# Kernel optimization log

Measured on AMD Instinct MI355X. Metric: run time of the kernel, lower is better.

The kernel has to match this reference:

```python
import jax, jax.numpy as jnp
import numpy as np

T, N = 512, 256          # timesteps, parallel envs
STATE, HID = 64, 128     # input features, GRU hidden size


def setup_inputs() -> dict:
    key = jax.random.key(0)
    k = jax.random.split(key, 6)
    inputs = jax.random.normal(k[0], (T * N, STATE), dtype=jnp.float32)
    hxs = jax.random.normal(k[1], (N, HID), dtype=jnp.float32)
    masks = (jax.random.uniform(k[2], (T * N, 1)) > 0.02).astype(jnp.float32)
    # GRU params (torch layout: gates ordered r, z, n; rows = 3*HID)
    weight_ih = jax.random.normal(k[3], (3 * HID, STATE), dtype=jnp.float32) * 0.1
    weight_hh = jax.random.normal(k[4], (3 * HID, HID), dtype=jnp.float32) * 0.1
    bias_ih = jnp.zeros((3 * HID,), dtype=jnp.float32)  # init.constant_(0)
    bias_hh = jnp.zeros((3 * HID,), dtype=jnp.float32)
    return {
        "inputs": inputs, "hxs": hxs, "masks": masks,
        "weight_ih": weight_ih, "weight_hh": weight_hh,
        "bias_ih": bias_ih, "bias_hh": bias_hh,
    }


def reference(inputs, hxs, masks, weight_ih, weight_hh, bias_ih, bias_hh):
    n, hid = hxs.shape
    t = inputs.shape[0] // n
    x = inputs.reshape(t, n, -1)       # (t, n, state)
    m = masks.reshape(t, n, 1)         # (t, n, 1)

    # Input-to-gate projections are mask-independent: precompute for all steps.
    gx = jnp.einsum('tns,gs->tng', x, weight_ih) + bias_ih  # (t, n, 3H)

    def step(h, xs):
        gx_t, m_t = xs
        h = h * m_t                                 # inline reset (fused; replaces chunk splitting)
        gh = h @ weight_hh.T + bias_hh              # (n, 3H)
        xr, xz, xn = jnp.split(gx_t, 3, axis=-1)
        hr, hz, hn = jnp.split(gh, 3, axis=-1)
        r = jax.nn.sigmoid(xr + hr)
        z = jax.nn.sigmoid(xz + hz)
        cand = jnp.tanh(xn + r * hn)
        h = (1.0 - z) * cand + z * h                # torch GRU update
        return h, h

    h_final, ys = jax.lax.scan(step, hxs, (gx, m))  # ys: (t, n, H)
    return ys.reshape(t * n, hid), h_final
```

## Files before the change

### kernel.cpp

```cpp
#include <hip/hip_runtime.h>
#include <math.h>

#define T_STEPS  512
#define N_ENVS   256
#define STATE    64
#define HID      128
#define NTHREADS 512

typedef _Float16 half8   __attribute__((ext_vector_type(8)));
typedef _Float16 half4_t __attribute__((ext_vector_type(4)));
typedef float    floatx4 __attribute__((ext_vector_type(4)));

__device__ __forceinline__ float sigmoid_fast(float v) {
    return __builtin_amdgcn_rcpf(1.f + __expf(-v));
}
__device__ __forceinline__ float tanh_fast(float v) {
    const float e  = __expf(-2.f * fabsf(v));
    const float mg = (1.f - e) * __builtin_amdgcn_rcpf(1.f + e);
    return copysignf(mg, v);
}

__global__ __launch_bounds__(NTHREADS, 2) void gru_mfma_split(
    const float* __restrict__ x,
    const float* __restrict__ h0,
    const float* __restrict__ masks,
    const float* __restrict__ wih,
    const float* __restrict__ whh,
    const float* __restrict__ bih,
    const float* __restrict__ bhh,
    float* __restrict__ out)
{
    const int b    = blockIdx.x;
    const int tid  = threadIdx.x;
    const int w    = tid >> 6;
    const int lane = tid & 63;
    const int c    = lane & 15;
    const int quad = lane >> 4;
    const int j    = 16 * w + c;

    __shared__ __align__(16) _Float16 buf[2][HID];
    __shared__ __align__(16) _Float16 xh[2][16][STATE];
    __shared__ __align__(16) float    gxp[16][HID][4];
    __shared__ __align__(16) float    ring[2][16][HID];
    __shared__ float ms[32];

    const int rowb[3] = { j, HID + j, 2 * HID + j };
    half8 Bh[3][4];
#pragma unroll
    for (int ti = 0; ti < 3; ++ti) {
        const int g = rowb[ti];
#pragma unroll
        for (int kt = 0; kt < 4; ++kt) {
            const float* src = whh + (size_t)g * HID + kt * 32 + quad * 8;
            const float4 p0 = *(const float4*)(src);
            const float4 p1 = *(const float4*)(src + 4);
            half8 hb;
            hb[0] = (_Float16)p0.x; hb[1] = (_Float16)p0.y;
            hb[2] = (_Float16)p0.z; hb[3] = (_Float16)p0.w;
            hb[4] = (_Float16)p1.x; hb[5] = (_Float16)p1.y;
            hb[6] = (_Float16)p1.z; hb[7] = (_Float16)p1.w;
            Bh[ti][kt] = hb;
        }
    }
    half8 Bx[3][2];
#pragma unroll
    for (int ti = 0; ti < 3; ++ti) {
        const int g = rowb[ti];
#pragma unroll
        for (int kt = 0; kt < 2; ++kt) {
            const float* src = wih + (size_t)g * STATE + kt * 32 + quad * 8;
            const float4 p0 = *(const float4*)(src);
            const float4 p1 = *(const float4*)(src + 4);
            half8 hb;
            hb[0] = (_Float16)p0.x; hb[1] = (_Float16)p0.y;
            hb[2] = (_Float16)p0.z; hb[3] = (_Float16)p0.w;
            hb[4] = (_Float16)p1.x; hb[5] = (_Float16)p1.y;
            hb[6] = (_Float16)p1.z; hb[7] = (_Float16)p1.w;
            Bx[ti][kt] = hb;
        }
    }

    const float br  = bih[j] + bhh[j];
    const float bz  = bih[HID + j] + bhh[HID + j];
    const float bhn = bhh[2 * HID + j];
    const float bxn = bih[2 * HID + j];

    float hr = h0[(size_t)b * HID + j];
    const float m0 = masks[b];
    float hm = m0 * hr;
    if (quad == 0) buf[0][j] = (_Float16)hm;

    float4 xp = {0.f, 0.f, 0.f, 0.f};
    if (tid < 256) {
        const int k = tid >> 4, cc = (tid & 15) * 4;
        const float4 xv = *(const float4*)(x + ((size_t)k * N_ENVS + b) * STATE + cc);
        half4_t hx = {(_Float16)xv.x, (_Float16)xv.y, (_Float16)xv.z, (_Float16)xv.w};
        *(half4_t*)&xh[0][k][cc] = hx;
        xp = *(const float4*)(x + ((size_t)(16 + k) * N_ENVS + b) * STATE + cc);
    }
    float mreg = 0.f;
    if (tid < 16) {
        ms[tid] = masks[(size_t)tid * N_ENVS + b];
        mreg = masks[(size_t)(16 + tid) * N_ENVS + b];
    }
    __syncthreads();

    const floatx4 zero4 = {0.f, 0.f, 0.f, 0.f};

    for (int tc = 0; tc < 32; ++tc) {
        if (tc > 0) {
            const int k = tid >> 5, jj = (tid & 31) * 4;
            *(float4*)(out + ((size_t)((tc - 1) * 16 + k) * N_ENVS + b) * HID + jj) =
                *(const float4*)&ring[(tc - 1) & 1][k][jj];
        }
        if (tid < 256) {
            const int k = tid >> 4, cc = (tid & 15) * 4;
            half4_t hx = {(_Float16)xp.x, (_Float16)xp.y, (_Float16)xp.z, (_Float16)xp.w};
            *(half4_t*)&xh[(tc + 1) & 1][k][cc] = hx;
            const int st = (tc + 2) * 16 + k;
            if (st < T_STEPS)
                xp = *(const float4*)(x + ((size_t)st * N_ENVS + b) * STATE + cc);
        }
        if (tid < 16) {
            ms[(tc * 16 + 16 + tid) & 31] = mreg;
            const int st = tc * 16 + 32 + tid;
            if (st < T_STEPS) mreg = masks[(size_t)st * N_ENVS + b];
        }

        {
            const _Float16* xr = &xh[tc & 1][c][0];
            half8 ax0 = *(const half8*)&xr[quad * 8];
            half8 ax1 = *(const half8*)&xr[32 + quad * 8];
            floatx4 g0 = __builtin_amdgcn_mfma_f32_16x16x32_f16(ax0, Bx[0][0], zero4, 0, 0, 0);
            floatx4 g1 = __builtin_amdgcn_mfma_f32_16x16x32_f16(ax0, Bx[1][0], zero4, 0, 0, 0);
            floatx4 g2 = __builtin_amdgcn_mfma_f32_16x16x32_f16(ax0, Bx[2][0], zero4, 0, 0, 0);
            g0 = __builtin_amdgcn_mfma_f32_16x16x32_f16(ax1, Bx[0][1], g0, 0, 0, 0);
            g1 = __builtin_amdgcn_mfma_f32_16x16x32_f16(ax1, Bx[1][1], g1, 0, 0, 0);
            g2 = __builtin_amdgcn_mfma_f32_16x16x32_f16(ax1, Bx[2][1], g2, 0, 0, 0);
#pragma unroll
            for (int i = 0; i < 4; ++i) {
                const int s4 = quad * 4 + i;
                gxp[s4][j][0] = g0[i];
                gxp[s4][j][1] = g1[i];
                gxp[s4][j][2] = g2[i];
            }
        }
        __syncthreads();

#pragma unroll
        for (int s = 0; s < 16; ++s) {
            const int t = tc * 16 + s;
            const _Float16* bufc = buf[s & 1];
            _Float16* bufn = (_Float16*)buf[(s + 1) & 1];

            half8 a0 = *(const half8*)(bufc + 0 * 32 + quad * 8);
            half8 a1 = *(const half8*)(bufc + 1 * 32 + quad * 8);
            half8 a2 = *(const half8*)(bufc + 2 * 32 + quad * 8);
            half8 a3 = *(const half8*)(bufc + 3 * 32 + quad * 8);

            floatx4 r_a = __builtin_amdgcn_mfma_f32_16x16x32_f16(a0, Bh[0][0], zero4, 0, 0, 0);
            floatx4 r_b = __builtin_amdgcn_mfma_f32_16x16x32_f16(a2, Bh[0][2], zero4, 0, 0, 0);
            floatx4 z_a = __builtin_amdgcn_mfma_f32_16x16x32_f16(a0, Bh[1][0], zero4, 0, 0, 0);
            floatx4 z_b = __builtin_amdgcn_mfma_f32_16x16x32_f16(a2, Bh[1][2], zero4, 0, 0, 0);
            floatx4 n_a = __builtin_amdgcn_mfma_f32_16x16x32_f16(a0, Bh[2][0], zero4, 0, 0, 0);
            floatx4 n_b = __builtin_amdgcn_mfma_f32_16x16x32_f16(a2, Bh[2][2], zero4, 0, 0, 0);
            r_a = __builtin_amdgcn_mfma_f32_16x16x32_f16(a1, Bh[0][1], r_a, 0, 0, 0);
            r_b = __builtin_amdgcn_mfma_f32_16x16x32_f16(a3, Bh[0][3], r_b, 0, 0, 0);
            z_a = __builtin_amdgcn_mfma_f32_16x16x32_f16(a1, Bh[1][1], z_a, 0, 0, 0);
            z_b = __builtin_amdgcn_mfma_f32_16x16x32_f16(a3, Bh[1][3], z_b, 0, 0, 0);
            n_a = __builtin_amdgcn_mfma_f32_16x16x32_f16(a1, Bh[2][1], n_a, 0, 0, 0);
            n_b = __builtin_amdgcn_mfma_f32_16x16x32_f16(a3, Bh[2][3], n_b, 0, 0, 0);

            const float4 gx4 = *(const float4*)&gxp[s][j][0];

            const float ur = (r_a[0] + r_b[0]) + gx4.x + br;
            const float uz = (z_a[0] + z_b[0]) + gx4.y + bz;
            const float hn = (n_a[0] + n_b[0]) + bhn;
            const float xn = gx4.z + bxn;
            const float r  = sigmoid_fast(ur);
            const float z  = sigmoid_fast(uz);
            const float cd = tanh_fast(fmaf(r, hn, xn));
            const float hnew = fmaf(z, hm - cd, cd);

            if (quad == 0) ring[tc & 1][s][j] = hnew;
            if (t < T_STEPS - 1) {
                const float mn = ms[(t + 1) & 31];
                hm = mn * hnew;
                if (quad == 0) bufn[j] = (_Float16)hm;
            }
            hr = hnew;
            __syncthreads();
        }
    }

    {
        const int k = tid >> 5, jj = (tid & 31) * 4;
        *(float4*)(out + ((size_t)(496 + k) * N_ENVS + b) * HID + jj) =
            *(const float4*)&ring[1][k][jj];
    }
    if (quad == 0)
        out[(size_t)T_STEPS * N_ENVS * HID + (size_t)b * HID + j] = hr;
}

extern "C" void kernel_launch(void* const* d_in, const int* in_sizes, int n_in,
                              void* d_out, int out_size, void* d_ws, size_t ws_size,
                              hipStream_t stream) {
    const float* x   = (const float*)d_in[0];
    const float* h0  = (const float*)d_in[1];
    const float* mk  = (const float*)d_in[2];
    const float* wih = (const float*)d_in[3];
    const float* whh = (const float*)d_in[4];
    const float* bih = (const float*)d_in[5];
    const float* bhh = (const float*)d_in[6];
    float* out = (float*)d_out;

    hipLaunchKernelGGL(gru_mfma_split, dim3(N_ENVS), dim3(NTHREADS), 0, stream,
                       x, h0, mk, wih, whh, bih, bhh, out);
}
```

Measured before the change: 305.1 us.

## Keep masks and outputs in registers, pack gate preacts to fp16, fuse activations

Masks move from shared memory into per-lane registers and are read with readlane, and the outputs are buffered in registers instead of an LDS ring. Each quad keeps its own four timesteps and writes them out per chunk with scalar stores. The input-gate preactivations are stored as fp16 with the biases folded in, halving LDS traffic. The xh rows are padded to reduce bank conflicts. The sigmoid/tanh/update sequence is fused into one reciprocal, shortening the serial per-step chain, at the cost of fp16 precision on the input gates and less coalesced output stores.

```diff
diff --git a/kernel.cpp b/kernel.cpp
--- a/kernel.cpp
+++ b/kernel.cpp
@@ -6,21 +6,13 @@
 #define STATE    64
 #define HID      128
 #define NTHREADS 512
+#define XPAD     72
 
 typedef _Float16 half8   __attribute__((ext_vector_type(8)));
 typedef _Float16 half4_t __attribute__((ext_vector_type(4)));
 typedef float    floatx4 __attribute__((ext_vector_type(4)));
 
-__device__ __forceinline__ float sigmoid_fast(float v) {
-    return __builtin_amdgcn_rcpf(1.f + __expf(-v));
-}
-__device__ __forceinline__ float tanh_fast(float v) {
-    const float e  = __expf(-2.f * fabsf(v));
-    const float mg = (1.f - e) * __builtin_amdgcn_rcpf(1.f + e);
-    return copysignf(mg, v);
-}
-
-__global__ __launch_bounds__(NTHREADS, 2) void gru_mfma_split(
+__global__ __launch_bounds__(NTHREADS, 2) void gru_r6(
     const float* __restrict__ x,
     const float* __restrict__ h0,
     const float* __restrict__ masks,
@@ -39,10 +31,8 @@
     const int j    = 16 * w + c;
 
     __shared__ __align__(16) _Float16 buf[2][HID];
-    __shared__ __align__(16) _Float16 xh[2][16][STATE];
-    __shared__ __align__(16) float    gxp[16][HID][4];
-    __shared__ __align__(16) float    ring[2][16][HID];
-    __shared__ float ms[32];
+    __shared__ __align__(16) _Float16 xh[2][16][XPAD];
+    __shared__ __align__(16) _Float16 gxp[16][HID][4];
 
     const int rowb[3] = { j, HID + j, 2 * HID + j };
     half8 Bh[3][4];
@@ -82,12 +72,11 @@
 
     const float br  = bih[j] + bhh[j];
     const float bz  = bih[HID + j] + bhh[HID + j];
+    const float bxn = bih[2 * HID + j];
     const float bhn = bhh[2 * HID + j];
-    const float bxn = bih[2 * HID + j];
 
     float hr = h0[(size_t)b * HID + j];
-    const float m0 = masks[b];
-    float hm = m0 * hr;
+    float hm = masks[b] * hr;
     if (quad == 0) buf[0][j] = (_Float16)hm;
 
     float4 xp = {0.f, 0.f, 0.f, 0.f};
@@ -98,20 +87,24 @@
         *(half4_t*)&xh[0][k][cc] = hx;
         xp = *(const float4*)(x + ((size_t)(16 + k) * N_ENVS + b) * STATE + cc);
     }
-    float mreg = 0.f;
-    if (tid < 16) {
-        ms[tid] = masks[(size_t)tid * N_ENVS + b];
-        mreg = masks[(size_t)(16 + tid) * N_ENVS + b];
-    }
+    float mwin  = masks[(size_t)(1  + (lane & 15)) * N_ENVS + b];
+    float mwin_nxt = masks[(size_t)(17 + (lane & 15)) * N_ENVS + b];
+
+    float o[4] = {0.f, 0.f, 0.f, 0.f};
+
     __syncthreads();
 
     const floatx4 zero4 = {0.f, 0.f, 0.f, 0.f};
 
     for (int tc = 0; tc < 32; ++tc) {
         if (tc > 0) {
-            const int k = tid >> 5, jj = (tid & 31) * 4;
-            *(float4*)(out + ((size_t)((tc - 1) * 16 + k) * N_ENVS + b) * HID + jj) =
-                *(const float4*)&ring[(tc - 1) & 1][k][jj];
+            const int tbp = (tc - 1) * 16;
+#pragma unroll
+            for (int i = 0; i < 4; ++i)
+                out[((size_t)(tbp + quad * 4 + i) * N_ENVS + b) * HID + j] = o[i];
+            mwin = mwin_nxt;
+            const int stm = (tc + 1) * 16 + 1 + (lane & 15);
+            mwin_nxt = masks[(size_t)(stm < T_STEPS ? stm : T_STEPS - 1) * N_ENVS + b];
         }
         if (tid < 256) {
             const int k = tid >> 4, cc = (tid & 15) * 4;
@@ -120,11 +113,6 @@
             const int st = (tc + 2) * 16 + k;
             if (st < T_STEPS)
                 xp = *(const float4*)(x + ((size_t)st * N_ENVS + b) * STATE + cc);
-        }
-        if (tid < 16) {
-            ms[(tc * 16 + 16 + tid) & 31] = mreg;
-            const int st = tc * 16 + 32 + tid;
-            if (st < T_STEPS) mreg = masks[(size_t)st * N_ENVS + b];
         }
 
         {
@@ -139,10 +127,12 @@
             g2 = __builtin_amdgcn_mfma_f32_16x16x32_f16(ax1, Bx[2][1], g2, 0, 0, 0);
 #pragma unroll
             for (int i = 0; i < 4; ++i) {
-                const int s4 = quad * 4 + i;
-                gxp[s4][j][0] = g0[i];
-                gxp[s4][j][1] = g1[i];
-                gxp[s4][j][2] = g2[i];
+                half4_t p;
+                p[0] = (_Float16)(g0[i] + br);
+                p[1] = (_Float16)(g1[i] + bz);
+                p[2] = (_Float16)(g2[i] + bxn);
+                p[3] = (_Float16)0.f;
+                *(half4_t*)&gxp[quad * 4 + i][j][0] = p;
             }
         }
         __syncthreads();
@@ -157,6 +147,7 @@
             half8 a1 = *(const half8*)(bufc + 1 * 32 + quad * 8);
             half8 a2 = *(const half8*)(bufc + 2 * 32 + quad * 8);
             half8 a3 = *(const half8*)(bufc + 3 * 32 + quad * 8);
+            const half4_t gxh = *(const half4_t*)&gxp[s][j][0];
 
             floatx4 r_a = __builtin_amdgcn_mfma_f32_16x16x32_f16(a0, Bh[0][0], zero4, 0, 0, 0);
             floatx4 r_b = __builtin_amdgcn_mfma_f32_16x16x32_f16(a2, Bh[0][2], zero4, 0, 0, 0);
@@ -171,20 +162,27 @@
             n_a = __builtin_amdgcn_mfma_f32_16x16x32_f16(a1, Bh[2][1], n_a, 0, 0, 0);
             n_b = __builtin_amdgcn_mfma_f32_16x16x32_f16(a3, Bh[2][3], n_b, 0, 0, 0);
 
-            const float4 gx4 = *(const float4*)&gxp[s][j][0];
-
-            const float ur = (r_a[0] + r_b[0]) + gx4.x + br;
-            const float uz = (z_a[0] + z_b[0]) + gx4.y + bz;
+            const float ur = (r_a[0] + r_b[0]) + (float)gxh[0];
+            const float uz = (z_a[0] + z_b[0]) + (float)gxh[1];
             const float hn = (n_a[0] + n_b[0]) + bhn;
-            const float xn = gx4.z + bxn;
-            const float r  = sigmoid_fast(ur);
-            const float z  = sigmoid_fast(uz);
-            const float cd = tanh_fast(fmaf(r, hn, xn));
-            const float hnew = fmaf(z, hm - cd, cd);
-
-            if (quad == 0) ring[tc & 1][s][j] = hnew;
+            const float xn = (float)gxh[2];
+
+            const float e_r = __expf(-ur);
+            const float r   = __builtin_amdgcn_rcpf(1.f + e_r);
+            const float a   = fmaf(r, hn, xn);
+            const float e_t = __expf(-2.f * fabsf(a));
+            const float e_z = __expf(-fmaxf(uz, -30.f));
+            const float opt = 1.f + e_t;
+            float num = copysignf(e_z * (1.f - e_t), a);
+            num = fmaf(hm, opt, num);
+            const float den = opt * (1.f + e_z);
+            const float hnew = num * __builtin_amdgcn_rcpf(den);
+
+            o[s & 3] = (quad == (s >> 2)) ? hnew : o[s & 3];
+
             if (t < T_STEPS - 1) {
-                const float mn = ms[(t + 1) & 31];
+                const int   mi = __builtin_amdgcn_readlane(__float_as_int(mwin), s);
+                const float mn = __int_as_float(mi);
                 hm = mn * hnew;
                 if (quad == 0) bufn[j] = (_Float16)hm;
             }
@@ -194,9 +192,10 @@
     }
 
     {
-        const int k = tid >> 5, jj = (tid & 31) * 4;
-        *(float4*)(out + ((size_t)(496 + k) * N_ENVS + b) * HID + jj) =
-            *(const float4*)&ring[1][k][jj];
+        const int tbp = 31 * 16;
+#pragma unroll
+        for (int i = 0; i < 4; ++i)
+            out[((size_t)(tbp + quad * 4 + i) * N_ENVS + b) * HID + j] = o[i];
     }
     if (quad == 0)
         out[(size_t)T_STEPS * N_ENVS * HID + (size_t)b * HID + j] = hr;
@@ -214,6 +213,6 @@
     const float* bhh = (const float*)d_in[6];
     float* out = (float*)d_out;
 
-    hipLaunchKernelGGL(gru_mfma_split, dim3(N_ENVS), dim3(NTHREADS), 0, stream,
+    hipLaunchKernelGGL(gru_r6, dim3(N_ENVS), dim3(NTHREADS), 0, stream,
                        x, h0, mk, wih, whh, bih, bhh, out);
 }
```

Measured after the change: 291.7 us. 1.05x faster.
